# Performance work log

Hardware: AMD Instinct MI355X
Metric: run time of the kernel (lower is better)

## Reference

```python
import jax, jax.numpy as jnp
import numpy as np

B, S, E = 2, 2048, 1024
H, HKV = 16, 4
D = E // H          # head_dim = 64
REP = H // HKV      # kv repeat factor = 4


def setup_inputs() -> dict:
    key = jax.random.key(0)
    ks = jax.random.split(key, 9)
    std = 0.02
    x = jax.random.normal(ks[0], (B, S, E), dtype=jnp.float32)
    # causal mask: True means masked (upper triangle, strictly above diagonal)
    mask = jnp.triu(jnp.ones((S, S), dtype=bool), k=1)
    wq_w = jax.random.normal(ks[1], (E, E), dtype=jnp.float32) * std
    wq_b = jax.random.normal(ks[2], (E,), dtype=jnp.float32) * std
    wk_w = jax.random.normal(ks[3], (HKV * D, E), dtype=jnp.float32) * std
    wk_b = jax.random.normal(ks[4], (HKV * D,), dtype=jnp.float32) * std
    wv_w = jax.random.normal(ks[5], (HKV * D, E), dtype=jnp.float32) * std
    wv_b = jax.random.normal(ks[6], (HKV * D,), dtype=jnp.float32) * std
    wo_w = jax.random.normal(ks[7], (E, E), dtype=jnp.float32) * std
    wo_b = jax.random.normal(ks[8], (E,), dtype=jnp.float32) * std
    return {"x": x, "mask": mask, "wq_w": wq_w, "wq_b": wq_b,
            "wk_w": wk_w, "wk_b": wk_b, "wv_w": wv_w, "wv_b": wv_b,
            "wo_w": wo_w, "wo_b": wo_b}


def reference(x, mask, wq_w, wq_b, wk_w, wk_b, wv_w, wv_b, wo_w, wo_b):
    b, s, e = x.shape
    # projections (torch Linear: x @ W.T + b)
    q = x @ wq_w.T + wq_b                       # [B,S,E]
    k = x @ wk_w.T + wk_b                       # [B,S,HKV*D]
    v = x @ wv_w.T + wv_b
    # q grouped by kv head: [B, HKV, REP, S, D]; k/v: [B, HKV, S, D]
    q = q.reshape(b, s, HKV, REP, D).transpose(0, 2, 3, 1, 4)
    k = k.reshape(b, s, HKV, D).transpose(0, 2, 1, 3)
    v = v.reshape(b, s, HKV, D).transpose(0, 2, 1, 3)
    scale = D ** (-0.5)
    # scores [B, HKV, REP, Sq, Skv] -- same math as physical repeat_kv
    scores = jnp.einsum('bgrsd,bgtd->bgrst', q, k) * scale
    scores = jnp.where(mask, -jnp.inf, scores)
    w = jax.nn.softmax(scores, axis=-1)
    ctx = jnp.einsum('bgrst,bgtd->bgrsd', w, v)  # [B,HKV,REP,S,D]
    ctx = ctx.transpose(0, 3, 1, 2, 4).reshape(b, s, e)
    return ctx @ wo_w.T + wo_b
```

## Files before the change

kernel.cpp:

```cpp
#include <hip/hip_runtime.h>


typedef __attribute__((ext_vector_type(8))) short bh8;
typedef __attribute__((ext_vector_type(4))) short sh4;
typedef __attribute__((ext_vector_type(4))) float fv4;
typedef __attribute__((ext_vector_type(2))) unsigned int uv2;

#define MFMA16 __builtin_amdgcn_mfma_f32_16x16x32_bf16

static __device__ __forceinline__ float fast_exp2(float x) {
  return __builtin_amdgcn_exp2f(x);
}
static __device__ __forceinline__ unsigned short f2bf(float f) {
  unsigned int u; __builtin_memcpy(&u, &f, 4);
  u += 0x7fffu + ((u >> 16) & 1u);
  return (unsigned short)(u >> 16);
}
static __device__ __forceinline__ unsigned int pack2(float a, float b) {
  return (unsigned int)(unsigned short)f2bf(a) |
         ((unsigned int)(unsigned short)f2bf(b) << 16);
}
static __device__ __forceinline__ void gload16(const short* g, short* l) {
  __builtin_amdgcn_global_load_lds(
      (const __attribute__((address_space(1))) void*)g,
      (__attribute__((address_space(3))) void*)l, 16, 0, 0);
}

static __device__ __forceinline__ bh8 pshuf(const float* p, int quad, int l16) {
  unsigned int u01 = pack2(p[0], p[1]);
  unsigned int u23 = pack2(p[2], p[3]);
  unsigned int u45 = pack2(p[4], p[5]);
  unsigned int u67 = pack2(p[6], p[7]);
  const int g0 = (((quad << 1)    ) & 3) * 16 + l16;
  const int g1 = (((quad << 1) + 1) & 3) * 16 + l16;
  unsigned int w0l = __shfl((int)u01, g0), w0h = __shfl((int)u45, g0);
  unsigned int w1l = __shfl((int)u23, g0), w1h = __shfl((int)u67, g0);
  unsigned int w2l = __shfl((int)u01, g1), w2h = __shfl((int)u45, g1);
  unsigned int w3l = __shfl((int)u23, g1), w3h = __shfl((int)u67, g1);
  const bool up = (quad & 2) != 0;
  union { unsigned int w[4]; bh8 v; } pu;
  pu.w[0] = up ? w0h : w0l;
  pu.w[1] = up ? w1h : w1l;
  pu.w[2] = up ? w2h : w2l;
  pu.w[3] = up ? w3h : w3l;
  return pu.v;
}

__global__ __launch_bounds__(256) void cvt_all(
    const float* __restrict__ x,  const float* __restrict__ wq,
    const float* __restrict__ wk, const float* __restrict__ wv,
    const float* __restrict__ wo,
    short* __restrict__ xb, short* __restrict__ wqkvb, short* __restrict__ wob)
{
  const int i = blockIdx.x * 256 + threadIdx.x;
  const float* src; short* dst; int j;
  if (i < 1048576)      { j = i;           src = x;  dst = xb; }
  else if (i < 1310720) { j = i - 1048576; src = wq; dst = wqkvb; }
  else if (i < 1376256) { j = i - 1310720; src = wk; dst = wqkvb + (size_t)1024 * 1024; }
  else if (i < 1441792) { j = i - 1376256; src = wv; dst = wqkvb + (size_t)1280 * 1024; }
  else                  { j = i - 1441792; src = wo; dst = wob; }
  const float4 v = ((const float4*)src)[j];
  sh4 o = { (short)f2bf(v.x), (short)f2bf(v.y),
            (short)f2bf(v.z), (short)f2bf(v.w) };
  ((sh4*)dst)[j] = o;
}

__global__ __launch_bounds__(128) void gemm_2w(
    const short* __restrict__ A, const short* __restrict__ W,
    const float* __restrict__ biasQ, const float* __restrict__ biasK,
    const float* __restrict__ biasV,
    short* __restrict__ Cq, short* __restrict__ Ck, short* __restrict__ Cvt,
    float* __restrict__ Cf,
    int M, int K, int S, int mode, float scaleQ)
{
  __shared__ short As[64 * 64];
  __shared__ short Bs[128 * 64];
  const int tid = threadIdx.x;
  const int wave = tid >> 6, lane = tid & 63;
  const int quad = lane >> 4, l16 = lane & 15;
  const int row0 = blockIdx.x * 64, col0 = blockIdx.y * 128;
  const int wc = wave * 64;

  fv4 acc[4][4] = {};

  const int srow8  = lane >> 3;
  const int schunk = (lane & 7) ^ srow8;
  const short* agB = A + (size_t)(row0 + wave * 32 + srow8) * K + schunk * 8;
  const short* bgB = W + (size_t)(col0 + wave * 64 + srow8) * K + schunk * 8;

  const int fsw = (l16 & 7);

  for (int k0 = 0; k0 < K; k0 += 64) {
    __syncthreads();
    #pragma unroll
    for (int g = 0; g < 4; g++)
      gload16(agB + (size_t)(g * 8) * K + k0, &As[(wave * 32 + g * 8) * 64]);
    #pragma unroll
    for (int g = 0; g < 8; g++)
      gload16(bgB + (size_t)(g * 8) * K + k0, &Bs[(wave * 64 + g * 8) * 64]);
    __syncthreads();
    #pragma unroll
    for (int ks = 0; ks < 2; ks++) {
      const int co = ((ks * 4 + quad) ^ fsw) * 8;
      bh8 af[4], bf[4];
      #pragma unroll
      for (int i = 0; i < 4; i++)
        af[i] = *(const bh8*)&As[(i * 16 + l16) * 64 + co];
      #pragma unroll
      for (int j = 0; j < 4; j++)
        bf[j] = *(const bh8*)&Bs[(wc + j * 16 + l16) * 64 + co];
      #pragma unroll
      for (int i = 0; i < 4; i++)
        #pragma unroll
        for (int j = 0; j < 4; j++)
          acc[i][j] = MFMA16(af[i], bf[j], acc[i][j], 0, 0, 0);
    }
  }

  const int cw0 = col0 + wc;
  if (mode == 2) {
    float bv[4];
    #pragma unroll
    for (int j = 0; j < 4; j++) bv[j] = biasQ[cw0 + j * 16 + l16];
    #pragma unroll
    for (int i = 0; i < 4; i++) {
      const int row = row0 + i * 16 + quad * 4;
      #pragma unroll
      for (int j = 0; j < 4; j++) {
        const int col = cw0 + j * 16 + l16;
        #pragma unroll
        for (int r = 0; r < 4; r++)
          Cf[(size_t)(row + r) * 1024 + col] = acc[i][j][r] + bv[j];
      }
    }
  } else if (cw0 < 1024) {
    float bv[4];
    #pragma unroll
    for (int j = 0; j < 4; j++) bv[j] = biasQ[cw0 + j * 16 + l16];
    #pragma unroll
    for (int i = 0; i < 4; i++) {
      const int row = row0 + i * 16 + quad * 4;
      #pragma unroll
      for (int j = 0; j < 4; j++) {
        const int col = cw0 + j * 16 + l16;
        #pragma unroll
        for (int r = 0; r < 4; r++)
          Cq[(size_t)(row + r) * 1024 + col] =
              (short)f2bf((acc[i][j][r] + bv[j]) * scaleQ);
      }
    }
  } else if (cw0 < 1280) {
    float bv[4];
    #pragma unroll
    for (int j = 0; j < 4; j++) bv[j] = biasK[cw0 + j * 16 + l16 - 1024];
    #pragma unroll
    for (int i = 0; i < 4; i++) {
      const int row = row0 + i * 16 + quad * 4;
      #pragma unroll
      for (int j = 0; j < 4; j++) {
        const int col = cw0 + j * 16 + l16 - 1024;
        #pragma unroll
        for (int r = 0; r < 4; r++)
          Ck[(size_t)(row + r) * 256 + col] = (short)f2bf(acc[i][j][r] + bv[j]);
      }
    }
  } else {
    float bv[4];
    #pragma unroll
    for (int j = 0; j < 4; j++) bv[j] = biasV[cw0 + j * 16 + l16 - 1280];
    const int b  = row0 / S;
    const int sb = row0 - b * S;
    #pragma unroll
    for (int i = 0; i < 4; i++) {
      const int s = sb + i * 16 + quad * 4;
      #pragma unroll
      for (int j = 0; j < 4; j++) {
        const int np = cw0 + j * 16 + l16 - 1280;
        sh4 v = { (short)f2bf(acc[i][j][0] + bv[j]),
                  (short)f2bf(acc[i][j][1] + bv[j]),
                  (short)f2bf(acc[i][j][2] + bv[j]),
                  (short)f2bf(acc[i][j][3] + bv[j]) };
        *(sh4*)(Cvt + ((size_t)(b * 256 + np)) * S + s) = v;
      }
    }
  }
}

__global__ __launch_bounds__(256) void gqa_attn(
    const short* __restrict__ Q,
    const short* __restrict__ Kg,
    const short* __restrict__ Vt,
    short* __restrict__ ctx)
{
  const int S = 2048, E = 1024, KVE = 256;
  __shared__ short Ks[2][4096];
  __shared__ short Vs[2][4096];
  __shared__ short P2[4][16 * 72];

  const int wave = threadIdx.x >> 6;
  const int lane = threadIdx.x & 63;
  const int quad = lane >> 4, l16 = lane & 15;
  const int bh = blockIdx.y;
  const int b = bh >> 4, h = bh & 15, kv = h >> 2;

  const short* Kb = Kg + (size_t)b * S * KVE + kv * 64;
  const short* Vb = Vt + ((size_t)(b * 4 + kv)) * 64 * S;
  short* Pw = &P2[wave][0];

  const int srow = lane >> 3;
  const int scg  = (lane & 7) ^ srow;

  const int kc0 = (quad ^ (l16 & 7)) * 8;
  const int kc1 = ((quad ^ 4) ^ (l16 & 7)) * 8;
  const int pwr = l16 * 72;

  auto stageKV = [&](int buf, int t0) {
    #pragma unroll
    for (int e = 0; e < 2; e++) {
      const int g = wave * 2 + e;
      const int row = g * 8 + srow;
      gload16(Kb + (size_t)(t0 + row) * KVE + scg * 8, &Ks[buf][g * 512]);
      gload16(Vb + (size_t)row * S + t0 + scg * 8,     &Vs[buf][g * 512]);
    }
  };

  for (int ph = 0; ph < 2; ph++) {
    const int j = ph ? (31 - (int)blockIdx.x) : (int)blockIdx.x;
    const int qblk0 = j * 64;
    const int q0 = qblk0 + wave * 16;

    const short* qrow = Q + (size_t)(b * S + q0 + l16) * E + h * 64 + quad * 8;
    bh8 qf0 = *(const bh8*)(qrow);
    bh8 qf1 = *(const bh8*)(qrow + 32);

    fv4 acc0{}, acc1{}, acc2{}, acc3{};
    float rs = 0.f;

    const int nInt = qblk0 >> 6;
    if (nInt > 0) {
      stageKV(0, 0);
      __syncthreads();
      for (int it = 0; it < nInt; it++) {
        const int cur = it & 1;
        if (it + 1 < nInt) stageKV(cur ^ 1, (it + 1) * 64);

        fv4 st[4] = {};
        #pragma unroll
        for (int i = 0; i < 4; i++) {
          const int tb = (i * 16 + l16) * 64;
          bh8 k0 = *(const bh8*)&Ks[cur][tb + kc0];
          bh8 k1 = *(const bh8*)&Ks[cur][tb + kc1];
          st[i] = MFMA16(k0, qf0, st[i], 0, 0, 0);
          st[i] = MFMA16(k1, qf1, st[i], 0, 0, 0);
        }
        #pragma unroll
        for (int i = 0; i < 4; i++) {
          float p0 = fast_exp2(st[i][0]);
          float p1 = fast_exp2(st[i][1]);
          float p2 = fast_exp2(st[i][2]);
          float p3 = fast_exp2(st[i][3]);
          rs += (p0 + p1) + (p2 + p3);
          uv2 u = { pack2(p0, p1), pack2(p2, p3) };
          *(uv2*)&Pw[pwr + i * 16 + quad * 4] = u;
        }
        bh8 pfA = *(const bh8*)&Pw[pwr + quad * 8];
        bh8 pfB = *(const bh8*)&Pw[pwr + 32 + quad * 8];
        #pragma unroll
        for (int dt = 0; dt < 4; dt++) {
          const int db = (dt * 16 + l16) * 64;
          bh8 v0 = *(const bh8*)&Vs[cur][db + kc0];
          bh8 v1 = *(const bh8*)&Vs[cur][db + kc1];
          fv4* a = dt == 0 ? &acc0 : dt == 1 ? &acc1 : dt == 2 ? &acc2 : &acc3;
          *a = MFMA16(v0, pfA, *a, 0, 0, 0);
          *a = MFMA16(v1, pfB, *a, 0, 0, 0);
        }
        __syncthreads();
      }
    }

    const int nk = q0 + 16;
    for (int t0 = qblk0; t0 < nk; t0 += 32) {
      fv4 st0{}, st1{};
      {
        const short* kr = Kb + (size_t)(t0 + l16) * KVE + quad * 8;
        bh8 k0 = *(const bh8*)(kr);
        bh8 k1 = *(const bh8*)(kr + 32);
        st0 = MFMA16(k0, qf0, st0, 0, 0, 0);
        st0 = MFMA16(k1, qf1, st0, 0, 0, 0);
      }
      const bool do2 = (t0 + 16) < nk;
      if (do2) {
        const short* kr = Kb + (size_t)(t0 + 16 + l16) * KVE + quad * 8;
        bh8 k0 = *(const bh8*)(kr);
        bh8 k1 = *(const bh8*)(kr + 32);
        st1 = MFMA16(k0, qf0, st1, 0, 0, 0);
        st1 = MFMA16(k1, qf1, st1, 0, 0, 0);
      }
      const int qg = q0 + l16;
      float p[8];
      #pragma unroll
      for (int r = 0; r < 4; r++) {
        const int t = t0 + quad * 4 + r;
        p[r]     = (t <= qg)               ? fast_exp2(st0[r]) : 0.f;
        p[4 + r] = (do2 && (t + 16) <= qg) ? fast_exp2(st1[r]) : 0.f;
      }
      #pragma unroll
      for (int i = 0; i < 8; i++) rs += p[i];

      bh8 pf = pshuf(p, quad, l16);
      const short* vr = Vb + (size_t)l16 * S + t0 + quad * 8;
      acc0 = MFMA16(*(const bh8*)(vr),          pf, acc0, 0, 0, 0);
      acc1 = MFMA16(*(const bh8*)(vr + 16 * S), pf, acc1, 0, 0, 0);
      acc2 = MFMA16(*(const bh8*)(vr + 32 * S), pf, acc2, 0, 0, 0);
      acc3 = MFMA16(*(const bh8*)(vr + 48 * S), pf, acc3, 0, 0, 0);
    }

    float lsum = rs;
    lsum += __shfl_xor(lsum, 16);
    lsum += __shfl_xor(lsum, 32);
    const float inv = 1.f / lsum;

    short* orow = ctx + (size_t)(b * S + q0 + l16) * E + h * 64 + quad * 4;
    sh4 o0 = { (short)f2bf(acc0[0] * inv), (short)f2bf(acc0[1] * inv),
               (short)f2bf(acc0[2] * inv), (short)f2bf(acc0[3] * inv) };
    sh4 o1 = { (short)f2bf(acc1[0] * inv), (short)f2bf(acc1[1] * inv),
               (short)f2bf(acc1[2] * inv), (short)f2bf(acc1[3] * inv) };
    sh4 o2 = { (short)f2bf(acc2[0] * inv), (short)f2bf(acc2[1] * inv),
               (short)f2bf(acc2[2] * inv), (short)f2bf(acc2[3] * inv) };
    sh4 o3 = { (short)f2bf(acc3[0] * inv), (short)f2bf(acc3[1] * inv),
               (short)f2bf(acc3[2] * inv), (short)f2bf(acc3[3] * inv) };
    *(sh4*)(orow)      = o0;
    *(sh4*)(orow + 16) = o1;
    *(sh4*)(orow + 32) = o2;
    *(sh4*)(orow + 48) = o3;
  }
}

extern "C" void kernel_launch(void* const* d_in, const int* in_sizes, int n_in,
                              void* d_out, int out_size, void* d_ws, size_t ws_size,
                              hipStream_t stream)
{
  const float* x    = (const float*)d_in[0];
  const float* wq_w = (const float*)d_in[2];
  const float* wq_b = (const float*)d_in[3];
  const float* wk_w = (const float*)d_in[4];
  const float* wk_b = (const float*)d_in[5];
  const float* wv_w = (const float*)d_in[6];
  const float* wv_b = (const float*)d_in[7];
  const float* wo_w = (const float*)d_in[8];
  const float* wo_b = (const float*)d_in[9];
  float* out = (float*)d_out;

  const int S = 2048, E = 1024, M = 2 * S;
  const float sl2e = 0.125f * 1.44269504f;

  char* ob = (char*)d_out;
  short* Qb   = (short*)(ob);
  short* Kbuf = (short*)(ob + (size_t)( 8 << 20));
  short* Vtb  = (short*)(ob + (size_t)(10 << 20));

  char* ws = (char*)d_ws;
  short* xb    = (short*)(ws);
  short* wqkvb = (short*)(ws + (size_t)( 8 << 20));
  short* wob   = (short*)(ws + (size_t)(11 << 20));
  short* Cx    = xb;

  cvt_all<<<dim3(6656), dim3(256), 0, stream>>>(x, wq_w, wk_w, wv_w, wo_w,
                                                xb, wqkvb, wob);
  gemm_2w<<<dim3(M / 64, 1536 / 128), dim3(128), 0, stream>>>(
      xb, wqkvb, wq_b, wk_b, wv_b, Qb, Kbuf, Vtb, nullptr, M, E, S, 0, sl2e);
  gqa_attn<<<dim3(16, 2 * 16), dim3(256), 0, stream>>>(Qb, Kbuf, Vtb, Cx);
  gemm_2w<<<dim3(M / 64, 1024 / 128), dim3(128), 0, stream>>>(
      Cx, wob, wo_b, nullptr, nullptr, nullptr, nullptr, nullptr, out,
      M, E, S, 2, 1.f);
}
```

Measured before the change: 183.4 us.

## Process two adjacent 64-row query blocks per workgroup sharing K/V tiles

Each workgroup now handles 128 contiguous query rows (two 64-row sub-blocks per wave) instead of two separate 64-row blocks from opposite ends in sequence. Every K/V tile staged into LDS is reused for both query sub-blocks, which roughly halves K/V staging traffic and barriers per unit of work. The trade-off is coarser causal load balancing, with block indices reversed so the longest blocks launch first, plus higher register pressure from two sets of accumulators. The kernel_launch grid must also change to 16 blocks in x, and that part is not visible here.

```diff
diff --git a/kernel.cpp b/kernel.cpp
--- a/kernel.cpp
+++ b/kernel.cpp
@@ -195,13 +195,17 @@
   const int S = 2048, E = 1024, KVE = 256;
   __shared__ short Ks[2][4096];
   __shared__ short Vs[2][4096];
-  __shared__ short P2[4][16 * 72];
+  __shared__ short P2[4][32 * 72];
 
   const int wave = threadIdx.x >> 6;
   const int lane = threadIdx.x & 63;
   const int quad = lane >> 4, l16 = lane & 15;
   const int bh = blockIdx.y;
   const int b = bh >> 4, h = bh & 15, kv = h >> 2;
+  const int j = 15 - (int)blockIdx.x;
+  const int Q0 = j * 128;
+  const int qa = Q0 + wave * 16;
+  const int qb = Q0 + 64 + wave * 16;
 
   const short* Kb = Kg + (size_t)b * S * KVE + kv * 64;
   const short* Vb = Vt + ((size_t)(b * 4 + kv)) * 64 * S;
@@ -209,10 +213,10 @@
 
   const int srow = lane >> 3;
   const int scg  = (lane & 7) ^ srow;
-
   const int kc0 = (quad ^ (l16 & 7)) * 8;
   const int kc1 = ((quad ^ 4) ^ (l16 & 7)) * 8;
-  const int pwr = l16 * 72;
+  const int pwrA = l16 * 72;
+  const int pwrB = (16 + l16) * 72;
 
   auto stageKV = [&](int buf, int t0) {
     #pragma unroll
@@ -224,62 +228,84 @@
     }
   };
 
-  for (int ph = 0; ph < 2; ph++) {
-    const int j = ph ? (31 - (int)blockIdx.x) : (int)blockIdx.x;
-    const int qblk0 = j * 64;
-    const int q0 = qblk0 + wave * 16;
-
-    const short* qrow = Q + (size_t)(b * S + q0 + l16) * E + h * 64 + quad * 8;
-    bh8 qf0 = *(const bh8*)(qrow);
-    bh8 qf1 = *(const bh8*)(qrow + 32);
-
-    fv4 acc0{}, acc1{}, acc2{}, acc3{};
-    float rs = 0.f;
-
-    const int nInt = qblk0 >> 6;
-    if (nInt > 0) {
-      stageKV(0, 0);
-      __syncthreads();
-      for (int it = 0; it < nInt; it++) {
-        const int cur = it & 1;
-        if (it + 1 < nInt) stageKV(cur ^ 1, (it + 1) * 64);
-
-        fv4 st[4] = {};
-        #pragma unroll
-        for (int i = 0; i < 4; i++) {
-          const int tb = (i * 16 + l16) * 64;
-          bh8 k0 = *(const bh8*)&Ks[cur][tb + kc0];
-          bh8 k1 = *(const bh8*)&Ks[cur][tb + kc1];
-          st[i] = MFMA16(k0, qf0, st[i], 0, 0, 0);
-          st[i] = MFMA16(k1, qf1, st[i], 0, 0, 0);
-        }
-        #pragma unroll
-        for (int i = 0; i < 4; i++) {
-          float p0 = fast_exp2(st[i][0]);
-          float p1 = fast_exp2(st[i][1]);
-          float p2 = fast_exp2(st[i][2]);
-          float p3 = fast_exp2(st[i][3]);
-          rs += (p0 + p1) + (p2 + p3);
-          uv2 u = { pack2(p0, p1), pack2(p2, p3) };
-          *(uv2*)&Pw[pwr + i * 16 + quad * 4] = u;
-        }
-        bh8 pfA = *(const bh8*)&Pw[pwr + quad * 8];
-        bh8 pfB = *(const bh8*)&Pw[pwr + 32 + quad * 8];
-        #pragma unroll
-        for (int dt = 0; dt < 4; dt++) {
-          const int db = (dt * 16 + l16) * 64;
-          bh8 v0 = *(const bh8*)&Vs[cur][db + kc0];
-          bh8 v1 = *(const bh8*)&Vs[cur][db + kc1];
-          fv4* a = dt == 0 ? &acc0 : dt == 1 ? &acc1 : dt == 2 ? &acc2 : &acc3;
-          *a = MFMA16(v0, pfA, *a, 0, 0, 0);
-          *a = MFMA16(v1, pfB, *a, 0, 0, 0);
-        }
-        __syncthreads();
-      }
-    }
-
-    const int nk = q0 + 16;
-    for (int t0 = qblk0; t0 < nk; t0 += 32) {
+  const short* qrowA = Q + (size_t)(b * S + qa + l16) * E + h * 64 + quad * 8;
+  const short* qrowB = Q + (size_t)(b * S + qb + l16) * E + h * 64 + quad * 8;
+  bh8 qfa0 = *(const bh8*)(qrowA);
+  bh8 qfa1 = *(const bh8*)(qrowA + 32);
+  bh8 qfb0 = *(const bh8*)(qrowB);
+  bh8 qfb1 = *(const bh8*)(qrowB + 32);
+
+  fv4 accA[4] = {}, accB[4] = {};
+  float rsA = 0.f, rsB = 0.f;
+
+  const int nSt = 2 * j + 1;
+  stageKV(0, 0);
+  __syncthreads();
+  for (int it = 0; it < nSt; it++) {
+    const int cur = it & 1;
+    if (it + 1 < nSt) stageKV(cur ^ 1, (it + 1) * 64);
+    const bool doA = (it < 2 * j);
+
+    fv4 stA[4] = {}, stB[4] = {};
+    #pragma unroll
+    for (int i = 0; i < 4; i++) {
+      const int tb = (i * 16 + l16) * 64;
+      bh8 k0 = *(const bh8*)&Ks[cur][tb + kc0];
+      bh8 k1 = *(const bh8*)&Ks[cur][tb + kc1];
+      stB[i] = MFMA16(k0, qfb0, stB[i], 0, 0, 0);
+      stB[i] = MFMA16(k1, qfb1, stB[i], 0, 0, 0);
+      if (doA) {
+        stA[i] = MFMA16(k0, qfa0, stA[i], 0, 0, 0);
+        stA[i] = MFMA16(k1, qfa1, stA[i], 0, 0, 0);
+      }
+    }
+    #pragma unroll
+    for (int i = 0; i < 4; i++) {
+      float p0 = fast_exp2(stB[i][0]);
+      float p1 = fast_exp2(stB[i][1]);
+      float p2 = fast_exp2(stB[i][2]);
+      float p3 = fast_exp2(stB[i][3]);
+      rsB += (p0 + p1) + (p2 + p3);
+      uv2 u = { pack2(p0, p1), pack2(p2, p3) };
+      *(uv2*)&Pw[pwrB + i * 16 + quad * 4] = u;
+    }
+    if (doA) {
+      #pragma unroll
+      for (int i = 0; i < 4; i++) {
+        float p0 = fast_exp2(stA[i][0]);
+        float p1 = fast_exp2(stA[i][1]);
+        float p2 = fast_exp2(stA[i][2]);
+        float p3 = fast_exp2(stA[i][3]);
+        rsA += (p0 + p1) + (p2 + p3);
+        uv2 u = { pack2(p0, p1), pack2(p2, p3) };
+        *(uv2*)&Pw[pwrA + i * 16 + quad * 4] = u;
+      }
+    }
+    bh8 pB0 = *(const bh8*)&Pw[pwrB + quad * 8];
+    bh8 pB1 = *(const bh8*)&Pw[pwrB + 32 + quad * 8];
+    bh8 pA0 = {}, pA1 = {};
+    if (doA) {
+      pA0 = *(const bh8*)&Pw[pwrA + quad * 8];
+      pA1 = *(const bh8*)&Pw[pwrA + 32 + quad * 8];
+    }
+    #pragma unroll
+    for (int dt = 0; dt < 4; dt++) {
+      const int db = (dt * 16 + l16) * 64;
+      bh8 v0 = *(const bh8*)&Vs[cur][db + kc0];
+      bh8 v1 = *(const bh8*)&Vs[cur][db + kc1];
+      accB[dt] = MFMA16(v0, pB0, accB[dt], 0, 0, 0);
+      accB[dt] = MFMA16(v1, pB1, accB[dt], 0, 0, 0);
+      if (doA) {
+        accA[dt] = MFMA16(v0, pA0, accA[dt], 0, 0, 0);
+        accA[dt] = MFMA16(v1, pA1, accA[dt], 0, 0, 0);
+      }
+    }
+    __syncthreads();
+  }
+
+  auto diag = [&](int q0, fv4* acc, float& rs, int t0, int nk,
+                  bh8 qf0, bh8 qf1) {
+    for (; t0 < nk; t0 += 32) {
       fv4 st0{}, st1{};
       {
         const short* kr = Kb + (size_t)(t0 + l16) * KVE + quad * 8;
@@ -309,31 +335,30 @@
 
       bh8 pf = pshuf(p, quad, l16);
       const short* vr = Vb + (size_t)l16 * S + t0 + quad * 8;
-      acc0 = MFMA16(*(const bh8*)(vr),          pf, acc0, 0, 0, 0);
-      acc1 = MFMA16(*(const bh8*)(vr + 16 * S), pf, acc1, 0, 0, 0);
-      acc2 = MFMA16(*(const bh8*)(vr + 32 * S), pf, acc2, 0, 0, 0);
-      acc3 = MFMA16(*(const bh8*)(vr + 48 * S), pf, acc3, 0, 0, 0);
-    }
-
+      acc[0] = MFMA16(*(const bh8*)(vr),          pf, acc[0], 0, 0, 0);
+      acc[1] = MFMA16(*(const bh8*)(vr + 16 * S), pf, acc[1], 0, 0, 0);
+      acc[2] = MFMA16(*(const bh8*)(vr + 32 * S), pf, acc[2], 0, 0, 0);
+      acc[3] = MFMA16(*(const bh8*)(vr + 48 * S), pf, acc[3], 0, 0, 0);
+    }
+  };
+  diag(qa, accA, rsA, Q0,      qa + 16, qfa0, qfa1);
+  diag(qb, accB, rsB, Q0 + 64, qb + 16, qfb0, qfb1);
+
+  auto epi = [&](int q0, fv4* acc, float rs) {
     float lsum = rs;
     lsum += __shfl_xor(lsum, 16);
     lsum += __shfl_xor(lsum, 32);
     const float inv = 1.f / lsum;
-
     short* orow = ctx + (size_t)(b * S + q0 + l16) * E + h * 64 + quad * 4;
-    sh4 o0 = { (short)f2bf(acc0[0] * inv), (short)f2bf(acc0[1] * inv),
-               (short)f2bf(acc0[2] * inv), (short)f2bf(acc0[3] * inv) };
-    sh4 o1 = { (short)f2bf(acc1[0] * inv), (short)f2bf(acc1[1] * inv),
-               (short)f2bf(acc1[2] * inv), (short)f2bf(acc1[3] * inv) };
-    sh4 o2 = { (short)f2bf(acc2[0] * inv), (short)f2bf(acc2[1] * inv),
-               (short)f2bf(acc2[2] * inv), (short)f2bf(acc2[3] * inv) };
-    sh4 o3 = { (short)f2bf(acc3[0] * inv), (short)f2bf(acc3[1] * inv),
-               (short)f2bf(acc3[2] * inv), (short)f2bf(acc3[3] * inv) };
-    *(sh4*)(orow)      = o0;
-    *(sh4*)(orow + 16) = o1;
-    *(sh4*)(orow + 32) = o2;
-    *(sh4*)(orow + 48) = o3;
-  }
+    #pragma unroll
+    for (int dt = 0; dt < 4; dt++) {
+      sh4 o = { (short)f2bf(acc[dt][0] * inv), (short)f2bf(acc[dt][1] * inv),
+                (short)f2bf(acc[dt][2] * inv), (short)f2bf(acc[dt][3] * inv) };
+      *(sh4*)(orow + dt * 16) = o;
+    }
+  };
+  epi(qa, accA, rsA);
+  epi(qb, accB, rsB);
 }
 
 extern "C" void kernel_launch(void* const* d_in, const int* in_sizes, int n_in,
```

New measurement: 207.9 us. +13.3%, slower.
